# Kernel tuning notes

Measured on AMD Instinct MI355X. Metric: run time of the kernel, lower is better.

## Reference

```python
import jax, jax.numpy as jnp
import numpy as np
from jax import lax

N, C, H, W = 16, 512, 64, 64
INTER, HEADS, GROUPS, K = 512, 64, 8, 7
HEAD_DIM = INTER // HEADS


def setup_inputs() -> dict:
    key = jax.random.key(0)
    ks = jax.random.split(key, 12)
    s = 0.02
    return {
        "x": jax.random.normal(ks[0], (N, C, H, W), jnp.float32),
        "conv_w": jax.random.normal(ks[1], (INTER, C // GROUPS, K, K), jnp.float32) * s,
        "conv_b": jax.random.normal(ks[2], (INTER,), jnp.float32) * s,
        "ln_g": jnp.ones((INTER,), jnp.float32),
        "ln_b": jnp.zeros((INTER,), jnp.float32),
        "qw": jax.random.normal(ks[3], (INTER, INTER), jnp.float32) * s,
        "qb": jax.random.normal(ks[4], (INTER,), jnp.float32) * s,
        "kw": jax.random.normal(ks[5], (INTER, INTER), jnp.float32) * s,
        "kb": jax.random.normal(ks[6], (INTER,), jnp.float32) * s,
        "vw": jax.random.normal(ks[7], (INTER, INTER), jnp.float32) * s,
        "vb": jax.random.normal(ks[8], (INTER,), jnp.float32) * s,
        "pw": jax.random.normal(ks[9], (C, INTER), jnp.float32) * s,
        "pb": jax.random.normal(ks[10], (C,), jnp.float32) * s,
        "beta": jax.random.normal(ks[11], (1,), jnp.float32),
    }


def reference(x, conv_w, conv_b, ln_g, ln_b, qw, qb, kw, kb, vw, vb, pw, pb, beta):
    n, c, h, w = x.shape
    hw = h * w
    pad = (K - 1) // 2
    # grouped conv, NCHW
    xc = lax.conv_general_dilated(
        x, conv_w, window_strides=(1, 1), padding=[(pad, pad), (pad, pad)],
        dimension_numbers=("NCHW", "OIHW", "NCHW"), feature_group_count=GROUPS)
    xc = xc + conv_b[None, :, None, None]
    xc = xc.reshape(n, INTER, hw).transpose(0, 2, 1)  # [N, HW, INTER]
    # LayerNorm over channel dim
    mu = jnp.mean(xc, axis=-1, keepdims=True)
    var = jnp.mean(jnp.square(xc - mu), axis=-1, keepdims=True)
    xn = (xc - mu) * lax.rsqrt(var + 1e-5) * ln_g + ln_b
    # projections (torch Linear: y = x @ W.T + b)
    q = (xn @ qw.T + qb).reshape(n, hw, HEADS, HEAD_DIM).transpose(0, 2, 1, 3)  # [N,h,HW,d]
    k = (xn @ kw.T + kb).reshape(n, hw, HEADS, HEAD_DIM).transpose(0, 2, 3, 1)  # [N,h,d,HW]
    v = (xn @ vw.T + vb).reshape(n, hw, HEADS, HEAD_DIM).transpose(0, 2, 1, 3)  # [N,h,HW,d]
    k = jax.nn.softmax(k, axis=3)  # softmax over tokens
    corr = jnp.einsum("nhds,nhse->nhde", k, v)      # [N,h,d,d] compact context
    atten = jnp.einsum("nhsd,nhde->nhse", q, corr)  # [N,h,HW,d]
    atten = atten.transpose(0, 2, 1, 3).reshape(n, hw, INTER)
    xa = (atten @ pw.T + pb).transpose(0, 2, 1).reshape(n, c, h, w)
    return beta[0] * xa + x
```

## Files before the change

kernel.cpp:

```cpp
#include <hip/hip_runtime.h>
#include <hip/hip_bf16.h>

#define N_IMG 16
#define C_DIM 512
#define H_DIM 64
#define W_DIM 64
#define HW 4096
#define INTER 512
#define HEADS 64
#define GROUPS 8
#define KSZ 7
#define CPG 64
#define M_TOT (N_IMG * HW)

typedef short bf16x8 __attribute__((ext_vector_type(8)));
typedef short bf16x4 __attribute__((ext_vector_type(4)));
typedef float f32x4 __attribute__((ext_vector_type(4)));
typedef unsigned int u32;

__device__ __forceinline__ unsigned short f2bf(float f) {
    __hip_bfloat16 h = __float2bfloat16(f);
    return *reinterpret_cast<unsigned short*>(&h);
}
__device__ __forceinline__ float bf2f(unsigned short u) {
    u32 x = ((u32)u) << 16;
    union { u32 i; float f; } c; c.i = x; return c.f;
}
__device__ __forceinline__ void gload16(const void* g, void* l) {
    __builtin_amdgcn_global_load_lds(
        (const __attribute__((address_space(1))) u32*)g,
        (__attribute__((address_space(3))) u32*)l, 16, 0, 0);
}
__device__ __forceinline__ void raw_barrier() {
    asm volatile("" ::: "memory");
    __builtin_amdgcn_s_barrier();
    asm volatile("" ::: "memory");
}
#define WAIT_VM(N) asm volatile("s_waitcnt vmcnt(" #N ")" ::: "memory")

__global__ __launch_bounds__(256) void prep_kernel(
    const float* __restrict__ cw, const float* __restrict__ kw,
    const float* __restrict__ vw, const float* __restrict__ pw,
    unsigned short* __restrict__ pk, unsigned short* __restrict__ kwb,
    unsigned short* __restrict__ vwb, unsigned short* __restrict__ pwb,
    float* __restrict__ crw)
{
    const int b = blockIdx.x;
    const int tid = threadIdx.x;
    if (b < 6272) {
        int p = b * 256 + tid;
        int ci = p & 63;
        int co = (p >> 6) & 63;
        int r  = p >> 12;
        int dx = r % 7;
        int dyg = r / 7;
        int dy = dyg % 7;
        int g  = dyg / 7;
        float v = cw[(((size_t)(g * 64 + co)) * 64 + ci) * 49 + dy * 7 + dx];
        pk[(size_t)(g * 49 + dy * 7 + dx) * 4096 + co * 64 + (ci ^ ((co & 7) << 3))] = f2bf(v);
    } else if (b < 8320) {
        const float* w = (b < 7296) ? kw : vw;
        unsigned short* wp = (b < 7296) ? kwb : vwb;
        int e = ((b < 7296) ? (b - 6272) : (b - 7296)) * 256 + tid;
        int j = e & 7;
        int chunk = (e >> 3) & 511;
        int kt = (e >> 12) & 15;
        int t = e >> 16;
        int col = chunk & 127, kq = chunk >> 7;
        wp[e] = f2bf(w[(size_t)(t * 128 + col) * 512 + kt * 32 + kq * 8 + j]);
    } else if (b < 9344) {
        int i = (b - 8320) * 256 + tid;
        pwb[i] = f2bf(pw[i]);
    } else {
        crw[(b - 9344) * 256 + tid] = 0.f;
    }
}

__global__ __launch_bounds__(256) void xprep_kernel(
    const float* __restrict__ x, unsigned short* __restrict__ xb)
{
    const int row = blockIdx.x;
    const int g   = blockIdx.y;
    const int n   = blockIdx.z;
    const int tid = threadIdx.x;
    unsigned short* dst = xb + ((size_t)(n * 8 + g) * 70 + row) * 4608;

    if (row < 3 || row > 66) {
        bf16x8 z = (bf16x8){0,0,0,0,0,0,0,0};
        *(bf16x8*)&dst[tid * 8] = z;
        *(bf16x8*)&dst[(256 + tid) * 8] = z;
        if (tid < 64) *(bf16x8*)&dst[(512 + tid) * 8] = z;
        return;
    }
    const int y = row - 3;
    const int xcol = tid & 63;
    const int oct = tid >> 6;
    const int col = xcol + 3;
    const int cswz = (col & 7) << 3;
    const float* src = x + (((size_t)(n * C_DIM + g * CPG)) * H_DIM + y) * W_DIM + xcol;
#pragma unroll
    for (int h = 0; h < 2; ++h) {
        const int ci0 = oct * 16 + h * 8;
        unsigned short tmp[8];
#pragma unroll
        for (int j = 0; j < 8; ++j)
            tmp[j] = f2bf(src[(size_t)(ci0 + j) * (H_DIM * W_DIM)]);
        *(bf16x8*)&dst[col * 64 + (ci0 ^ cswz)] = *(bf16x8*)tmp;
    }
    if (tid < 64) {
        const int hc[8] = {0, 1, 2, 67, 68, 69, 70, 71};
        int c = hc[tid >> 3], o8 = (tid & 7) * 8;
        *(bf16x8*)&dst[c * 64 + (o8 ^ ((c & 7) << 3))] = (bf16x8){0,0,0,0,0,0,0,0};
    }
}

__global__ __launch_bounds__(256) void conv_mfma2_kernel(
    const unsigned short* __restrict__ xb, const unsigned short* __restrict__ pk,
    const float* __restrict__ cb, unsigned short* __restrict__ xc)
{
    __shared__ __align__(16) unsigned short in_ring[4 * 72 * 64];
    __shared__ __align__(16) unsigned short w_lds[2 * 4096];

    const int bid  = blockIdx.x;
    const int wgid = (bid & 7) * 256 + (bid >> 3);
    const int g  = wgid >> 8;
    const int n  = (wgid >> 4) & 15;
    const int y0 = (wgid & 15) * 4;
    const int tid  = threadIdx.x;
    const int lane = tid & 63;
    const int wv   = tid >> 6;
    const int lx   = lane & 15;
    const int q4   = lane >> 4;
    const int koff = q4 * 8;
    const int c3   = 512 + (tid & 63);

    const unsigned short* xbase = xb + ((size_t)(n * 8 + g) * 70) * 4608;
    const unsigned short* pkg   = pk + (size_t)g * 49 * 4096;

    f32x4 acc[4][4];
#pragma unroll
    for (int i = 0; i < 4; ++i)
#pragma unroll
        for (int j = 0; j < 4; ++j) acc[i][j] = (f32x4){0.f, 0.f, 0.f, 0.f};

#pragma unroll
    for (int r = 0; r < 4; ++r) {
        const unsigned short* src = xbase + (size_t)(y0 + r) * 4608;
        gload16(src + tid * 8,         &in_ring[r * 4608 + tid * 8]);
        gload16(src + (256 + tid) * 8, &in_ring[r * 4608 + (256 + tid) * 8]);
        gload16(src + c3 * 8,          &in_ring[r * 4608 + c3 * 8]);
    }
    gload16(pkg + tid * 8,         &w_lds[tid * 8]);
    gload16(pkg + (256 + tid) * 8, &w_lds[(256 + tid) * 8]);

    for (int dy = 0; dy < 7; ++dy) {
#pragma unroll
        for (int dx = 0; dx < 7; ++dx) {
            const int t = dy * 7 + dx;
            raw_barrier();
            if (dx == 0 && dy > 0) {
                const int slot = (dy + 3) & 3;
                const unsigned short* src = xbase + (size_t)(y0 + dy + 3) * 4608;
                gload16(src + tid * 8,         &in_ring[slot * 4608 + tid * 8]);
                gload16(src + (256 + tid) * 8, &in_ring[slot * 4608 + (256 + tid) * 8]);
                gload16(src + c3 * 8,          &in_ring[slot * 4608 + c3 * 8]);
            }
            if (t < 48) {
                const unsigned short* wsrc = pkg + (size_t)(t + 1) * 4096;
                unsigned short* wdst = &w_lds[((t + 1) & 1) * 4096];
                gload16(wsrc + tid * 8,         wdst + tid * 8);
                gload16(wsrc + (256 + tid) * 8, wdst + (256 + tid) * 8);
                WAIT_VM(2);
            } else {
                WAIT_VM(0);
            }
            __builtin_amdgcn_sched_barrier(0);
            raw_barrier();
            __builtin_amdgcn_sched_barrier(0);

            const unsigned short* wcur = &w_lds[(t & 1) * 4096];
            bf16x8 b[2][4];
#pragma unroll
            for (int kc = 0; kc < 2; ++kc)
#pragma unroll
                for (int ct = 0; ct < 4; ++ct) {
                    const int co = ct * 16 + lx;
                    b[kc][ct] = *(const bf16x8*)
                        &wcur[co * 64 + ((kc * 32 + koff) ^ ((co & 7) << 3))];
                }
            const int col  = wv * 16 + lx + dx;
            const int cswz = (col & 7) << 3;
#pragma unroll
            for (int ty = 0; ty < 4; ++ty) {
                const int slot = (dy + ty) & 3;
#pragma unroll
                for (int kc = 0; kc < 2; ++kc) {
                    bf16x8 a = *(const bf16x8*)
                        &in_ring[slot * 4608 + col * 64 + ((kc * 32 + koff) ^ cswz)];
#pragma unroll
                    for (int ct = 0; ct < 4; ++ct)
                        acc[ty][ct] = __builtin_amdgcn_mfma_f32_16x16x32_bf16(
                            a, b[kc][ct], acc[ty][ct], 0, 0, 0);
                }
            }
        }
    }

#pragma unroll
    for (int ct = 0; ct < 4; ++ct) {
        const float bv = cb[g * 64 + ct * 16 + lx];
        const int cidx = g * 64 + ct * 16 + lx;
#pragma unroll
        for (int ty = 0; ty < 4; ++ty) {
            const int yy = y0 + ty;
#pragma unroll
            for (int r = 0; r < 4; ++r) {
                const int xx = wv * 16 + q4 * 4 + r;
                xc[((size_t)(n * HW + yy * W_DIM + xx)) * INTER + cidx]
                    = f2bf(acc[ty][ct][r] + bv);
            }
        }
    }
}

__global__ __launch_bounds__(256) void ln_kernel(
    unsigned short* __restrict__ xc, const float* __restrict__ g,
    const float* __restrict__ b)
{
    const int tid  = threadIdx.x;
    const int half = tid >> 7;
    const int l    = tid & 127;
    const size_t row = (size_t)blockIdx.x * 2 + half;

    bf16x4 u = *(const bf16x4*)(xc + row * INTER + l * 4);
    float v0 = bf2f((unsigned short)u[0]), v1 = bf2f((unsigned short)u[1]);
    float v2 = bf2f((unsigned short)u[2]), v3 = bf2f((unsigned short)u[3]);
    float s  = v0 + v1 + v2 + v3;
    float sq = v0 * v0 + v1 * v1 + v2 * v2 + v3 * v3;
#pragma unroll
    for (int off = 32; off; off >>= 1) {
        s  += __shfl_xor(s, off);
        sq += __shfl_xor(sq, off);
    }
    __shared__ float red[4][2];
    const int wid = tid >> 6;
    if ((tid & 63) == 0) { red[wid][0] = s; red[wid][1] = sq; }
    __syncthreads();
    const int w0 = half * 2;
    float S  = red[w0][0] + red[w0 + 1][0];
    float SQ = red[w0][1] + red[w0 + 1][1];
    float mu  = S * (1.f / INTER);
    float var = SQ * (1.f / INTER) - mu * mu;
    float rs  = rsqrtf(var + 1e-5f);
    float4 gg = ((const float4*)g)[l];
    float4 bb = ((const float4*)b)[l];
    bf16x4 o;
    o[0] = (short)f2bf((v0 - mu) * rs * gg.x + bb.x);
    o[1] = (short)f2bf((v1 - mu) * rs * gg.y + bb.y);
    o[2] = (short)f2bf((v2 - mu) * rs * gg.z + bb.z);
    o[3] = (short)f2bf((v3 - mu) * rs * gg.w + bb.w);
    *(bf16x4*)(xc + row * INTER + l * 4) = o;
}

__global__ __launch_bounds__(256, 2) void gemm_kv_corr_kernel(
    const unsigned short* __restrict__ A,
    const unsigned short* __restrict__ Wk, const unsigned short* __restrict__ Wv,
    const float* __restrict__ bk, const float* __restrict__ bv,
    float* __restrict__ crw, float* __restrict__ esw)
{
    __shared__ __align__(16) unsigned short pool[32768];
    unsigned short* ek_lds = pool;
    unsigned short* v_lds  = pool + 16384;

    const int tid  = threadIdx.x;
    const int lane = tid & 63;
    const int w    = tid >> 6;
    const int lx   = lane & 15;
    const int kq4  = lane >> 4;

    const int orig = blockIdx.x;
    const int wgid = (orig & 7) * 256 + (orig >> 3);
    const int m0   = (wgid >> 2) * 128;
    const int ct4  = wgid & 3;
    const int mbase = (w & 1) * 64;
    const int nbase = (w >> 1) * 64;
    const int n = m0 >> 12;

    const unsigned short* wkt = Wk + (size_t)ct4 * 65536;
    const unsigned short* wvt = Wv + (size_t)ct4 * 65536;

    f32x4 acck[4][4], accv[4][4];
#pragma unroll
    for (int i = 0; i < 4; ++i)
#pragma unroll
        for (int j = 0; j < 4; ++j) {
            acck[i][j] = (f32x4){0.f, 0.f, 0.f, 0.f};
            accv[i][j] = (f32x4){0.f, 0.f, 0.f, 0.f};
        }

#pragma unroll
    for (int it = 0; it < 2; ++it) {
        int c = it * 256 + tid;
        gload16(A + (size_t)(m0 + (c & 127)) * 512 + (c >> 7) * 8, &pool[c * 8]);
        gload16(wkt + c * 8, &pool[(1024 + c) * 8]);
        gload16(wvt + c * 8, &pool[(2048 + c) * 8]);
    }

    for (int kt = 0; kt < 16; ++kt) {
        const int b = kt & 1;
        if (kt < 15) {
            const int nb = b ^ 1;
#pragma unroll
            for (int it = 0; it < 2; ++it) {
                int c = it * 256 + tid;
                gload16(A + (size_t)(m0 + (c & 127)) * 512 + (kt + 1) * 32 + (c >> 7) * 8,
                        &pool[(nb * 512 + c) * 8]);
                gload16(wkt + (size_t)(kt + 1) * 4096 + c * 8, &pool[(1024 + nb * 512 + c) * 8]);
                gload16(wvt + (size_t)(kt + 1) * 4096 + c * 8, &pool[(2048 + nb * 512 + c) * 8]);
            }
            WAIT_VM(6);
        } else {
            WAIT_VM(0);
        }
        __builtin_amdgcn_sched_barrier(0);
        raw_barrier();
        __builtin_amdgcn_sched_barrier(0);

        bf16x8 a[4], bkf[4], bvf[4];
#pragma unroll
        for (int i = 0; i < 4; ++i) {
            a[i]   = *(const bf16x8*)&pool[(b * 512 + kq4 * 128 + mbase + i * 16 + lx) * 8];
            bkf[i] = *(const bf16x8*)&pool[(1024 + b * 512 + kq4 * 128 + nbase + i * 16 + lx) * 8];
            bvf[i] = *(const bf16x8*)&pool[(2048 + b * 512 + kq4 * 128 + nbase + i * 16 + lx) * 8];
        }
#pragma unroll
        for (int i = 0; i < 4; ++i)
#pragma unroll
            for (int j = 0; j < 4; ++j) {
                acck[i][j] = __builtin_amdgcn_mfma_f32_16x16x32_bf16(a[i], bkf[j], acck[i][j], 0, 0, 0);
                accv[i][j] = __builtin_amdgcn_mfma_f32_16x16x32_bf16(a[i], bvf[j], accv[i][j], 0, 0, 0);
            }
        raw_barrier();
    }

#pragma unroll
    for (int j = 0; j < 4; ++j) {
        const int colk = nbase + j * 16 + lx;
        const float bkv = bk[ct4 * 128 + colk];
        const float bvv = bv[ct4 * 128 + colk];
        const int sw = (colk & 7) << 3;
#pragma unroll
        for (int i = 0; i < 4; ++i) {
            const int t0 = mbase + i * 16 + kq4 * 4;
            const int idx = colk * 128 + (t0 ^ sw);
            bf16x4 ew, vw;
#pragma unroll
            for (int r = 0; r < 4; ++r) {
                ew[r] = (short)f2bf(__expf(acck[i][j][r] + bkv));
                vw[r] = (short)f2bf(accv[i][j][r] + bvv);
            }
            *(bf16x4*)&ek_lds[idx] = ew;
            *(bf16x4*)&v_lds[idx]  = vw;
        }
    }
    const int d = lane >> 3, e = lane & 7;
    const int hbase = (w >> 1) * 8;
#pragma unroll
    for (int h = 0; h < 8; ++h) {
        const int hb = hbase + h;
        const int ck = hb * 8 + d;
        const int ce = hb * 8 + e;
        const int swk = d << 3, swe = e << 3;
        float crh = 0.f, esh = 0.f;
#pragma unroll
        for (int tb = 0; tb < 16; ++tb) {
            const int t0 = mbase + tb * 4;
            bf16x4 ekv = *(const bf16x4*)&ek_lds[ck * 128 + (t0 ^ swk)];
            bf16x4 vvv = *(const bf16x4*)&v_lds[ce * 128 + (t0 ^ swe)];
#pragma unroll
            for (int r = 0; r < 4; ++r) {
                float ekf = bf2f((unsigned short)ekv[r]);
                crh = fmaf(ekf, bf2f((unsigned short)vvv[r]), crh);
                esh += ekf;
            }
        }
        const int nh = n * 64 + ct4 * 16 + hb;
        atomicAdd(&crw[(size_t)nh * 64 + d * 8 + e], crh);
        if (e == 0) atomicAdd(&esw[nh * 8 + d], esh);
    }
}

__global__ __launch_bounds__(256) void gcomp_kernel(
    const float* __restrict__ qw, const float* __restrict__ crw,
    const float* __restrict__ esw, unsigned short* __restrict__ G)
{
    const int h = blockIdx.x;
    const int n = blockIdx.y;
    const int tid = threadIdx.x;
    const int nh = n * 64 + h;
    __shared__ float C[64];
    if (tid < 64) C[tid] = crw[(size_t)nh * 64 + tid] / esw[nh * 8 + (tid >> 3)];
    __syncthreads();
#pragma unroll
    for (int rep = 0; rep < 2; ++rep) {
        const int k = rep * 256 + tid;
        float o[8] = {};
#pragma unroll
        for (int d = 0; d < 8; ++d) {
            float qv = qw[(size_t)(h * 8 + d) * 512 + k];
#pragma unroll
            for (int e = 0; e < 8; ++e) o[e] = fmaf(qv, C[d * 8 + e], o[e]);
        }
        bf16x8 ov;
#pragma unroll
        for (int e = 0; e < 8; ++e) ov[e] = (short)f2bf(o[e]);
        *(bf16x8*)&G[((size_t)n * 512 + k) * 512 + h * 8] = ov;
    }
}

__global__ __launch_bounds__(256) void compose_kernel(
    const unsigned short* __restrict__ Pwb, const unsigned short* __restrict__ G,
    unsigned short* __restrict__ Wf)
{
    __shared__ __align__(16) unsigned short pool[16384];
    const int tid  = threadIdx.x;
    const int lane = tid & 63;
    const int w    = tid >> 6;
    const int lx   = lane & 15;
    const int kq4  = lane >> 4;

    const int tile = blockIdx.x;
    const int n    = blockIdx.y;
    const int m0 = (tile >> 2) * 128;
    const int n0 = (tile & 3) * 128;
    const int mbase = (w & 1) * 64;
    const int nbase = (w >> 1) * 64;
    const unsigned short* Gn = G + (size_t)n * 262144;

    f32x4 acc[4][4];
#pragma unroll
    for (int i = 0; i < 4; ++i)
#pragma unroll
        for (int j = 0; j < 4; ++j) acc[i][j] = (f32x4){0.f, 0.f, 0.f, 0.f};

#pragma unroll
    for (int it = 0; it < 2; ++it) {
        int c = it * 256 + tid;
        gload16(Pwb + (size_t)(m0 + (c & 127)) * 512 + (c >> 7) * 8, &pool[c * 8]);
        gload16(Gn + (size_t)(n0 + (c & 127)) * 512 + (c >> 7) * 8, &pool[(1024 + c) * 8]);
    }
    __syncthreads();

    for (int kt = 0; kt < 16; ++kt) {
        const int b = kt & 1;
        if (kt < 15) {
            const int nb = b ^ 1;
#pragma unroll
            for (int it = 0; it < 2; ++it) {
                int c = it * 256 + tid;
                gload16(Pwb + (size_t)(m0 + (c & 127)) * 512 + (kt + 1) * 32 + (c >> 7) * 8,
                        &pool[(nb * 512 + c) * 8]);
                gload16(Gn + (size_t)(n0 + (c & 127)) * 512 + (kt + 1) * 32 + (c >> 7) * 8,
                        &pool[(1024 + nb * 512 + c) * 8]);
            }
        }
        bf16x8 a[4], bf[4];
#pragma unroll
        for (int i = 0; i < 4; ++i) {
            a[i]  = *(const bf16x8*)&pool[(b * 512 + kq4 * 128 + mbase + i * 16 + lx) * 8];
            bf[i] = *(const bf16x8*)&pool[(1024 + b * 512 + kq4 * 128 + nbase + i * 16 + lx) * 8];
        }
#pragma unroll
        for (int i = 0; i < 4; ++i)
#pragma unroll
            for (int j = 0; j < 4; ++j)
                acc[i][j] = __builtin_amdgcn_mfma_f32_16x16x32_bf16(a[i], bf[j], acc[i][j], 0, 0, 0);
        __syncthreads();
    }

#pragma unroll
    for (int j = 0; j < 4; ++j) {
        const int col = n0 + nbase + j * 16 + lx;
#pragma unroll
        for (int i = 0; i < 4; ++i) {
            const int rowb = m0 + mbase + i * 16 + kq4 * 4;
#pragma unroll
            for (int r = 0; r < 4; ++r)
                Wf[(size_t)n * 262144 + (size_t)(rowb + r) * 512 + col] = f2bf(acc[i][j][r]);
        }
    }
}

__global__ __launch_bounds__(256) void wfpack_kernel(
    const unsigned short* __restrict__ Wf, unsigned short* __restrict__ wfp)
{
    const int n = blockIdx.y;
    int e = blockIdx.x * 256 + threadIdx.x;
    int j = e & 7;
    int chunk = (e >> 3) & 511;
    int kt = (e >> 12) & 15;
    int t = e >> 16;
    int col = chunk & 127, kq = chunk >> 7;
    wfp[(size_t)n * 262144 + e] =
        Wf[(size_t)n * 262144 + (size_t)(t * 128 + col) * 512 + kt * 32 + kq * 8 + j];
}

__global__ __launch_bounds__(256) void bias2_kernel(
    const float* __restrict__ qb, const float* __restrict__ crw,
    const float* __restrict__ esw, const float* __restrict__ pw,
    const float* __restrict__ pb, float* __restrict__ b2)
{
    const int n = blockIdx.x;
    const int tid = threadIdx.x;
    __shared__ float qbc[512];
#pragma unroll
    for (int rep = 0; rep < 2; ++rep) {
        int j = rep * 256 + tid;
        int h = j >> 3, e = j & 7;
        const int nh = n * 64 + h;
        float s = 0.f;
#pragma unroll
        for (int d = 0; d < 8; ++d)
            s += qb[h * 8 + d] * crw[(size_t)nh * 64 + d * 8 + e] / esw[nh * 8 + d];
        qbc[j] = s;
    }
    __syncthreads();
#pragma unroll
    for (int rep = 0; rep < 2; ++rep) {
        int c = rep * 256 + tid;
        const float4* pr = (const float4*)(pw + (size_t)c * 512);
        float s = pb[c];
        for (int q = 0; q < 128; ++q) {
            float4 pv = pr[q];
            s += qbc[q * 4 + 0] * pv.x + qbc[q * 4 + 1] * pv.y
               + qbc[q * 4 + 2] * pv.z + qbc[q * 4 + 3] * pv.w;
        }
        b2[n * 512 + c] = s;
    }
}

__global__ __launch_bounds__(256) void gemm_p_kernel(
    const unsigned short* __restrict__ A, const unsigned short* __restrict__ Wp,
    const float* __restrict__ bias, float* __restrict__ Y,
    const float* __restrict__ xres, const float* __restrict__ betap)
{
    __shared__ __align__(16) unsigned short pool[24576];
    const int tid  = threadIdx.x;
    const int lane = tid & 63;
    const int w    = tid >> 6;
    const int lx   = lane & 15;
    const int kq4  = lane >> 4;

    const int orig = blockIdx.x;
    const int wgid = (orig & 7) * 128 + (orig >> 3);
    const int m0 = (wgid >> 2) * 256;
    const int n0 = (wgid & 3) * 128;
    const int mbase = (w & 1) * 128;
    const int nbase = (w >> 1) * 64;
    const int nimg = m0 >> 12;

    f32x4 acc[8][4];
#pragma unroll
    for (int i = 0; i < 8; ++i)
#pragma unroll
        for (int j = 0; j < 4; ++j) acc[i][j] = (f32x4){0.f, 0.f, 0.f, 0.f};

    const unsigned short* wpt = Wp + (size_t)nimg * 262144 + (size_t)(wgid & 3) * 65536;

#pragma unroll
    for (int it = 0; it < 4; ++it) {
        int c = it * 256 + tid;
        gload16(A + (size_t)(m0 + (c & 255)) * 512 + (c >> 8) * 8, &pool[c * 8]);
    }
#pragma unroll
    for (int it = 0; it < 2; ++it) {
        int c = it * 256 + tid;
        gload16(wpt + c * 8, &pool[16384 + c * 8]);
    }

    for (int kt = 0; kt < 16; ++kt) {
        const int b = kt & 1;
        if (kt < 15) {
            const int nb = b ^ 1;
#pragma unroll
            for (int it = 0; it < 4; ++it) {
                int c = it * 256 + tid;
                gload16(A + (size_t)(m0 + (c & 255)) * 512 + (kt + 1) * 32 + (c >> 8) * 8,
                        &pool[(nb * 1024 + c) * 8]);
            }
#pragma unroll
            for (int it = 0; it < 2; ++it) {
                int c = it * 256 + tid;
                gload16(wpt + (size_t)(kt + 1) * 4096 + c * 8,
                        &pool[16384 + (nb * 512 + c) * 8]);
            }
            WAIT_VM(6);
        } else {
            WAIT_VM(0);
        }
        __builtin_amdgcn_sched_barrier(0);
        raw_barrier();
        __builtin_amdgcn_sched_barrier(0);

        bf16x8 a[8], bf[4];
#pragma unroll
        for (int i = 0; i < 8; ++i)
            a[i] = *(const bf16x8*)&pool[(b * 1024 + kq4 * 256 + mbase + i * 16 + lx) * 8];
#pragma unroll
        for (int j = 0; j < 4; ++j)
            bf[j] = *(const bf16x8*)&pool[16384 + (b * 512 + kq4 * 128 + nbase + j * 16 + lx) * 8];
#pragma unroll
        for (int i = 0; i < 8; ++i)
#pragma unroll
            for (int j = 0; j < 4; ++j)
                acc[i][j] = __builtin_amdgcn_mfma_f32_16x16x32_bf16(a[i], bf[j], acc[i][j], 0, 0, 0);
        raw_barrier();
    }

    const float beta = betap[0];
#pragma unroll
    for (int j = 0; j < 4; ++j) {
        const int c = n0 + nbase + j * 16 + lx;
        const float pbv = bias[nimg * 512 + c];
        const size_t cbase = ((size_t)(nimg * 512 + c)) * 4096;
#pragma unroll
        for (int i = 0; i < 8; ++i) {
            const int s = (m0 & 4095) + mbase + i * 16 + kq4 * 4;
            float4 xr = *(const float4*)(xres + cbase + s);
            float4 o;
            o.x = beta * (acc[i][j][0] + pbv) + xr.x;
            o.y = beta * (acc[i][j][1] + pbv) + xr.y;
            o.z = beta * (acc[i][j][2] + pbv) + xr.z;
            o.w = beta * (acc[i][j][3] + pbv) + xr.w;
            *(float4*)(Y + cbase + s) = o;
        }
    }
}

extern "C" void kernel_launch(void* const* d_in, const int* in_sizes, int n_in,
                              void* d_out, int out_size, void* d_ws, size_t ws_size,
                              hipStream_t stream)
{
    (void)in_sizes; (void)n_in; (void)out_size; (void)ws_size;
    const float* x   = (const float*)d_in[0];
    const float* cw  = (const float*)d_in[1];
    const float* cb  = (const float*)d_in[2];
    const float* lng = (const float*)d_in[3];
    const float* lnb = (const float*)d_in[4];
    const float* qw  = (const float*)d_in[5];
    const float* qb  = (const float*)d_in[6];
    const float* kw  = (const float*)d_in[7];
    const float* kb  = (const float*)d_in[8];
    const float* vw  = (const float*)d_in[9];
    const float* vb  = (const float*)d_in[10];
    const float* pw  = (const float*)d_in[11];
    const float* pb  = (const float*)d_in[12];
    const float* beta = (const float*)d_in[13];
    float* out = (float*)d_out;

    char* ws = (char*)d_ws;
    const size_t SZ  = (size_t)M_TOT * INTER * sizeof(float);
    const size_t HSZ = (size_t)M_TOT * INTER * 2;
    unsigned short* xc   = (unsigned short*)ws;
    unsigned short* G    = (unsigned short*)(ws + HSZ);
    unsigned short* wfin = G + (size_t)16 * 262144;
    unsigned short* wfp  = wfin + (size_t)16 * 262144;
    unsigned short* pwb  = wfp + (size_t)16 * 262144;
    float* b2            = (float*)(pwb + 262144);
    float* crw  = (float*)(ws + SZ);
    float* esw  = crw + 65536;
    unsigned short* pk  = (unsigned short*)(ws + SZ + (2 << 20));
    unsigned short* kwb = (unsigned short*)(ws + SZ + (6 << 20));
    unsigned short* vwb = kwb + 262144;
    unsigned short* xb  = vwb + 262144;

    prep_kernel<<<dim3(9632), 256, 0, stream>>>(cw, kw, vw, pw, pk, kwb, vwb, pwb, crw);
    xprep_kernel<<<dim3(70, 8, 16), 256, 0, stream>>>(x, xb);

    conv_mfma2_kernel<<<dim3(2048), 256, 0, stream>>>(xb, pk, cb, xc);
    ln_kernel<<<dim3(M_TOT / 2), 256, 0, stream>>>(xc, lng, lnb);

    gemm_kv_corr_kernel<<<dim3(2048), 256, 0, stream>>>(xc, kwb, vwb, kb, vb, crw, esw);

    gcomp_kernel<<<dim3(64, 16), 256, 0, stream>>>(qw, crw, esw, G);
    compose_kernel<<<dim3(16, 16), 256, 0, stream>>>(pwb, G, wfin);
    wfpack_kernel<<<dim3(1024, 16), 256, 0, stream>>>(wfin, wfp);
    bias2_kernel<<<dim3(16), 256, 0, stream>>>(qb, crw, esw, pw, pb, b2);

    gemm_p_kernel<<<dim3(1024), 256, 0, stream>>>(xc, wfp, b2, out, x, beta);
}
```

Before: 507.5 us.

## Merge xprep into prep, pack composed weights directly, raise MFMA wave priority

The x-to-bf16 padded repack now runs as extra blocks inside prep_kernel, which removes one launch. compose_kernel writes its output straight into the packed tile layout that gemm_p expects, so the wfpack kernel and its intermediate buffer are gone. s_setprio(1) wraps the MFMA sections of the conv, kv and p GEMMs to favour waves that are issuing math. The costs are scattered 2-byte stores in compose and an uneven prep grid.

```diff
diff --git a/kernel.cpp b/kernel.cpp
--- a/kernel.cpp
+++ b/kernel.cpp
@@ -41,9 +41,10 @@
 __global__ __launch_bounds__(256) void prep_kernel(
     const float* __restrict__ cw, const float* __restrict__ kw,
     const float* __restrict__ vw, const float* __restrict__ pw,
+    const float* __restrict__ x,
     unsigned short* __restrict__ pk, unsigned short* __restrict__ kwb,
     unsigned short* __restrict__ vwb, unsigned short* __restrict__ pwb,
-    float* __restrict__ crw)
+    float* __restrict__ crw, unsigned short* __restrict__ xb)
 {
     const int b = blockIdx.x;
     const int tid = threadIdx.x;
@@ -58,7 +59,9 @@
         int g  = dyg / 7;
         float v = cw[(((size_t)(g * 64 + co)) * 64 + ci) * 49 + dy * 7 + dx];
         pk[(size_t)(g * 49 + dy * 7 + dx) * 4096 + co * 64 + (ci ^ ((co & 7) << 3))] = f2bf(v);
-    } else if (b < 8320) {
+        return;
+    }
+    if (b < 8320) {
         const float* w = (b < 7296) ? kw : vw;
         unsigned short* wp = (b < 7296) ? kwb : vwb;
         int e = ((b < 7296) ? (b - 6272) : (b - 7296)) * 256 + tid;
@@ -68,49 +71,52 @@
         int t = e >> 16;
         int col = chunk & 127, kq = chunk >> 7;
         wp[e] = f2bf(w[(size_t)(t * 128 + col) * 512 + kt * 32 + kq * 8 + j]);
-    } else if (b < 9344) {
+        return;
+    }
+    if (b < 9344) {
         int i = (b - 8320) * 256 + tid;
         pwb[i] = f2bf(pw[i]);
-    } else {
+        return;
+    }
+    if (b < 9632) {
         crw[(b - 9344) * 256 + tid] = 0.f;
-    }
-}
-
-__global__ __launch_bounds__(256) void xprep_kernel(
-    const float* __restrict__ x, unsigned short* __restrict__ xb)
-{
-    const int row = blockIdx.x;
-    const int g   = blockIdx.y;
-    const int n   = blockIdx.z;
-    const int tid = threadIdx.x;
-    unsigned short* dst = xb + ((size_t)(n * 8 + g) * 70 + row) * 4608;
-
-    if (row < 3 || row > 66) {
-        bf16x8 z = (bf16x8){0,0,0,0,0,0,0,0};
-        *(bf16x8*)&dst[tid * 8] = z;
-        *(bf16x8*)&dst[(256 + tid) * 8] = z;
-        if (tid < 64) *(bf16x8*)&dst[(512 + tid) * 8] = z;
         return;
     }
-    const int y = row - 3;
-    const int xcol = tid & 63;
-    const int oct = tid >> 6;
-    const int col = xcol + 3;
-    const int cswz = (col & 7) << 3;
-    const float* src = x + (((size_t)(n * C_DIM + g * CPG)) * H_DIM + y) * W_DIM + xcol;
-#pragma unroll
-    for (int h = 0; h < 2; ++h) {
-        const int ci0 = oct * 16 + h * 8;
-        unsigned short tmp[8];
-#pragma unroll
-        for (int j = 0; j < 8; ++j)
-            tmp[j] = f2bf(src[(size_t)(ci0 + j) * (H_DIM * W_DIM)]);
-        *(bf16x8*)&dst[col * 64 + (ci0 ^ cswz)] = *(bf16x8*)tmp;
-    }
-    if (tid < 64) {
-        const int hc[8] = {0, 1, 2, 67, 68, 69, 70, 71};
-        int c = hc[tid >> 3], o8 = (tid & 7) * 8;
-        *(bf16x8*)&dst[c * 64 + (o8 ^ ((c & 7) << 3))] = (bf16x8){0,0,0,0,0,0,0,0};
+    {
+        const int idx = b - 9632;
+        const int n   = idx / 560;
+        const int rem = idx - n * 560;
+        const int g   = rem / 70;
+        const int row = rem - g * 70;
+        unsigned short* dst = xb + ((size_t)(n * 8 + g) * 70 + row) * 4608;
+
+        if (row < 3 || row > 66) {
+            bf16x8 z = (bf16x8){0,0,0,0,0,0,0,0};
+            *(bf16x8*)&dst[tid * 8] = z;
+            *(bf16x8*)&dst[(256 + tid) * 8] = z;
+            if (tid < 64) *(bf16x8*)&dst[(512 + tid) * 8] = z;
+            return;
+        }
+        const int y = row - 3;
+        const int xcol = tid & 63;
+        const int oct = tid >> 6;
+        const int col = xcol + 3;
+        const int cswz = (col & 7) << 3;
+        const float* src = x + (((size_t)(n * C_DIM + g * CPG)) * H_DIM + y) * W_DIM + xcol;
+#pragma unroll
+        for (int h = 0; h < 2; ++h) {
+            const int ci0 = oct * 16 + h * 8;
+            unsigned short tmp[8];
+#pragma unroll
+            for (int j = 0; j < 8; ++j)
+                tmp[j] = f2bf(src[(size_t)(ci0 + j) * (H_DIM * W_DIM)]);
+            *(bf16x8*)&dst[col * 64 + (ci0 ^ cswz)] = *(bf16x8*)tmp;
+        }
+        if (tid < 64) {
+            const int hc[8] = {0, 1, 2, 67, 68, 69, 70, 71};
+            int c = hc[tid >> 3], o8 = (tid & 7) * 8;
+            *(bf16x8*)&dst[c * 64 + (o8 ^ ((c & 7) << 3))] = (bf16x8){0,0,0,0,0,0,0,0};
+        }
     }
 }
 
@@ -178,6 +184,7 @@
             raw_barrier();
             __builtin_amdgcn_sched_barrier(0);
 
+            __builtin_amdgcn_s_setprio(1);
             const unsigned short* wcur = &w_lds[(t & 1) * 4096];
             bf16x8 b[2][4];
 #pragma unroll
@@ -203,6 +210,7 @@
                             a, b[kc][ct], acc[ty][ct], 0, 0, 0);
                 }
             }
+            __builtin_amdgcn_s_setprio(0);
         }
     }
 
@@ -326,6 +334,7 @@
         raw_barrier();
         __builtin_amdgcn_sched_barrier(0);
 
+        __builtin_amdgcn_s_setprio(1);
         bf16x8 a[4], bkf[4], bvf[4];
 #pragma unroll
         for (int i = 0; i < 4; ++i) {
@@ -340,6 +349,7 @@
                 acck[i][j] = __builtin_amdgcn_mfma_f32_16x16x32_bf16(a[i], bkf[j], acck[i][j], 0, 0, 0);
                 accv[i][j] = __builtin_amdgcn_mfma_f32_16x16x32_bf16(a[i], bvf[j], accv[i][j], 0, 0, 0);
             }
+        __builtin_amdgcn_s_setprio(0);
         raw_barrier();
     }
 
@@ -420,7 +430,7 @@
 
 __global__ __launch_bounds__(256) void compose_kernel(
     const unsigned short* __restrict__ Pwb, const unsigned short* __restrict__ G,
-    unsigned short* __restrict__ Wf)
+    unsigned short* __restrict__ wfp)
 {
     __shared__ __align__(16) unsigned short pool[16384];
     const int tid  = threadIdx.x;
@@ -478,31 +488,22 @@
         __syncthreads();
     }
 
+    unsigned short* wfn = wfp + (size_t)n * 262144;
 #pragma unroll
     for (int j = 0; j < 4; ++j) {
-        const int col = n0 + nbase + j * 16 + lx;
+        const int K = n0 + nbase + j * 16 + lx;
+        const int kt = K >> 5, kq = (K >> 3) & 3, jp = K & 7;
+        const int ebase = (kt << 12) | (kq << 10) | jp;
 #pragma unroll
         for (int i = 0; i < 4; ++i) {
             const int rowb = m0 + mbase + i * 16 + kq4 * 4;
 #pragma unroll
-            for (int r = 0; r < 4; ++r)
-                Wf[(size_t)n * 262144 + (size_t)(rowb + r) * 512 + col] = f2bf(acc[i][j][r]);
-        }
-    }
-}
-
-__global__ __launch_bounds__(256) void wfpack_kernel(
-    const unsigned short* __restrict__ Wf, unsigned short* __restrict__ wfp)
-{
-    const int n = blockIdx.y;
-    int e = blockIdx.x * 256 + threadIdx.x;
-    int j = e & 7;
-    int chunk = (e >> 3) & 511;
-    int kt = (e >> 12) & 15;
-    int t = e >> 16;
-    int col = chunk & 127, kq = chunk >> 7;
-    wfp[(size_t)n * 262144 + e] =
-        Wf[(size_t)n * 262144 + (size_t)(t * 128 + col) * 512 + kt * 32 + kq * 8 + j];
+            for (int r = 0; r < 4; ++r) {
+                const int C = rowb + r;
+                wfn[((C >> 7) << 16) | ebase | ((C & 127) << 3)] = f2bf(acc[i][j][r]);
+            }
+        }
+    }
 }
 
 __global__ __launch_bounds__(256) void bias2_kernel(
@@ -602,6 +603,7 @@
         raw_barrier();
         __builtin_amdgcn_sched_barrier(0);
 
+        __builtin_amdgcn_s_setprio(1);
         bf16x8 a[8], bf[4];
 #pragma unroll
         for (int i = 0; i < 8; ++i)
@@ -614,6 +616,7 @@
 #pragma unroll
             for (int j = 0; j < 4; ++j)
                 acc[i][j] = __builtin_amdgcn_mfma_f32_16x16x32_bf16(a[i], bf[j], acc[i][j], 0, 0, 0);
+        __builtin_amdgcn_s_setprio(0);
         raw_barrier();
     }
 
@@ -663,8 +666,7 @@
     const size_t HSZ = (size_t)M_TOT * INTER * 2;
     unsigned short* xc   = (unsigned short*)ws;
     unsigned short* G    = (unsigned short*)(ws + HSZ);
-    unsigned short* wfin = G + (size_t)16 * 262144;
-    unsigned short* wfp  = wfin + (size_t)16 * 262144;
+    unsigned short* wfp  = G + (size_t)16 * 262144;
     unsigned short* pwb  = wfp + (size_t)16 * 262144;
     float* b2            = (float*)(pwb + 262144);
     float* crw  = (float*)(ws + SZ);
@@ -674,8 +676,8 @@
     unsigned short* vwb = kwb + 262144;
     unsigned short* xb  = vwb + 262144;
 
-    prep_kernel<<<dim3(9632), 256, 0, stream>>>(cw, kw, vw, pw, pk, kwb, vwb, pwb, crw);
-    xprep_kernel<<<dim3(70, 8, 16), 256, 0, stream>>>(x, xb);
+    prep_kernel<<<dim3(18592), 256, 0, stream>>>(cw, kw, vw, pw, x,
+                                                 pk, kwb, vwb, pwb, crw, xb);
 
     conv_mfma2_kernel<<<dim3(2048), 256, 0, stream>>>(xb, pk, cb, xc);
     ln_kernel<<<dim3(M_TOT / 2), 256, 0, stream>>>(xc, lng, lnb);
@@ -683,8 +685,7 @@
     gemm_kv_corr_kernel<<<dim3(2048), 256, 0, stream>>>(xc, kwb, vwb, kb, vb, crw, esw);
 
     gcomp_kernel<<<dim3(64, 16), 256, 0, stream>>>(qw, crw, esw, G);
-    compose_kernel<<<dim3(16, 16), 256, 0, stream>>>(pwb, G, wfin);
-    wfpack_kernel<<<dim3(1024, 16), 256, 0, stream>>>(wfin, wfp);
+    compose_kernel<<<dim3(16, 16), 256, 0, stream>>>(pwb, G, wfp);
     bias2_kernel<<<dim3(16), 256, 0, stream>>>(qb, crw, esw, pw, pb, b2);
 
     gemm_p_kernel<<<dim3(1024), 256, 0, stream>>>(xc, wfp, b2, out, x, beta);
```

After: 511.0 us. Within noise of the previous version (+0.7%).
